# Kernel optimization log

Hardware: AMD Instinct MI355X
Metric: run time of the kernel (lower is better)

## Reference

```python
import jax, jax.numpy as jnp
import numpy as np

N = 2048      # feature_num (nodes/sensors)
T = 5         # timd_num (window length)
D = 64        # embed_dim
TOPK = 21     # topk + 1 (includes self, cos(i,i)=1)
B = 32        # batch
EPS = 1e-5
NEG_SLOPE = 0.2


def setup_inputs() -> dict:
    key = jax.random.key(0)
    ks = jax.random.split(key, 9)
    s = 1.0 / np.sqrt(D)
    return {
        "x": jax.random.normal(ks[0], (B, N, T), jnp.float32),
        "emb": jax.random.normal(ks[1], (N, D), jnp.float32) * s,      # embedding table
        "W": jax.random.normal(ks[2], (D, T), jnp.float32) * (1.0 / np.sqrt(T)),  # GNN lin weight
        "Wb": jax.random.normal(ks[3], (D,), jnp.float32) * 0.01,       # GNN lin bias
        "a_src": jax.random.normal(ks[4], (2 * D,), jnp.float32) * s,   # attention vec (source half)
        "a_dst": jax.random.normal(ks[5], (2 * D,), jnp.float32) * s,   # attention vec (dest half)
        "gamma": jnp.ones((D,), jnp.float32),                            # BatchNorm1d weight
        "beta": jnp.zeros((D,), jnp.float32),                            # BatchNorm1d bias
        "fc_w": jax.random.normal(ks[6], (1, D), jnp.float32) * s,      # fc weight
        "fc_b": jnp.zeros((1,), jnp.float32),                            # fc bias
    }


def reference(x, emb, W, Wb, a_src, a_dst, gamma, beta, fc_w, fc_b):
    # --- cosine-sim topk graph build ---
    norm = jnp.linalg.norm(emb, axis=-1)                    # [N]
    cos = (emb @ emb.T) / (norm[:, None] * norm[None, :])   # [N,N]
    _, idx = jax.lax.top_k(cos, TOPK)                       # [N,TOPK]
    # scatter one-hot adjacency (vectorized, no per-row loop)
    adj = jnp.zeros((N, N), x.dtype).at[jnp.arange(N)[:, None], idx].set(1.0)
    # --- GNN: GDN-style attention message passing ---
    h = jnp.einsum('bnt,dt->bnd', x, W) + Wb                # [B,N,D]
    g = jnp.concatenate([h, jnp.broadcast_to(emb, h.shape)], axis=-1)  # [B,N,2D]
    e_src = g @ a_src                                       # [B,N]
    e_dst = g @ a_dst                                       # [B,N]
    e = jax.nn.leaky_relu(e_src[:, :, None] + e_dst[:, None, :], NEG_SLOPE)  # [B,N,N]
    e = jnp.where(adj > 0, e, jnp.float32(-1e9))
    alpha = jax.nn.softmax(e, axis=-1)                      # [B,N,N], rows sum to 1 over TOPK nbrs
    z = jax.nn.relu(jnp.einsum('bij,bjd->bid', alpha, h))   # [B,N,D]
    # --- output head: z * emb, BN over channels, relu, fc ---
    out = z * emb                                           # [B,N,D]
    mean = out.mean(axis=(0, 1))                            # BN1d stats over (batch, nodes)
    var = out.var(axis=(0, 1))
    out = (out - mean) * jax.lax.rsqrt(var + EPS) * gamma + beta
    out = jax.nn.relu(out)
    out = out @ fc_w.T + fc_b                               # [B,N,1]
    return out.reshape(-1, N)                               # [B,N]
```

## Files before the change

kernel.cpp:

```cpp
#include <hip/hip_runtime.h>
#include <math.h>

#define N_NODES 2048
#define T_WIN 5
#define D_EMB 64
#define TOPK 21
#define B_BATCH 32
#define BN_TOTAL (B_BATCH * N_NODES)
#define EPS_BN 1e-5f
#define NEG_SLOPE 0.2f
#define STATS_STRIDE 16

typedef unsigned long long u64;

__device__ __forceinline__ float wave_sum(float v) {
#pragma unroll
    for (int off = 32; off > 0; off >>= 1) v += __shfl_xor(v, off, 64);
    return v;
}

__device__ __forceinline__ u64 max64(u64 a, u64 b) { return a > b ? a : b; }
__device__ __forceinline__ u64 min64(u64 a, u64 b) { return a < b ? a : b; }

__device__ __forceinline__ u64 bitonic_sort64_desc(u64 key, int lane) {
#pragma unroll
    for (int k = 2; k <= 64; k <<= 1) {
#pragma unroll
        for (int j = k >> 1; j >= 1; j >>= 1) {
            u64 pk = __shfl_xor(key, j, 64);
            bool dirDesc = ((lane & k) == 0);
            bool keepMax = (((lane & j) == 0) == dirDesc);
            key = keepMax ? max64(key, pk) : min64(key, pk);
        }
    }
    return key;
}

__device__ __forceinline__ u64 bitonic_merge_top64(u64 a, u64 b, int lane) {
    u64 br = __shfl(b, 63 - lane, 64);
    u64 c = max64(a, br);
#pragma unroll
    for (int j = 32; j >= 1; j >>= 1) {
        u64 pk = __shfl_xor(c, j, 64);
        bool keepMax = ((lane & j) == 0);
        c = keepMax ? max64(c, pk) : min64(c, pk);
    }
    return c;
}

__global__ __launch_bounds__(256) void k_edge(
    const float* __restrict__ x, const float* __restrict__ W,
    const float* __restrict__ Wb, const float* __restrict__ a_src,
    const float* __restrict__ a_dst, const float* __restrict__ emb,
    float* __restrict__ es2T, float* __restrict__ ed2T,
    float* __restrict__ norms, float* __restrict__ stats,
    float* __restrict__ stats2) {
    if (blockIdx.x < 2) {
        float* p = blockIdx.x ? stats2 : stats;
        ((float4*)p)[threadIdx.x] = make_float4(0.f, 0.f, 0.f, 0.f);
    }
    int wid = threadIdx.x >> 6, lane = threadIdx.x & 63;
    int gw = blockIdx.x * 4 + wid;
    const float* wp = W + lane * T_WIN;
    float w0 = wp[0], w1 = wp[1], w2 = wp[2], w3 = wp[3], w4 = wp[4];
    float bias = Wb[lane];
    float as = a_src[lane], asE = a_src[D_EMB + lane];
    float ad = a_dst[lane], adE = a_dst[D_EMB + lane];

    for (int node = gw; node < BN_TOTAL; node += 8192) {
        int n = node & (N_NODES - 1);
        const float* xp = x + (size_t)node * T_WIN;
        float hv = bias + xp[0] * w0 + xp[1] * w1 + xp[2] * w2 + xp[3] * w3 + xp[4] * w4;
        float e = emb[n * D_EMB + lane];
        if (node < N_NODES) {
            float s2 = wave_sum(e * e);
            if (lane == 0) norms[node] = sqrtf(s2);
        }
        float es = wave_sum(hv * as + e * asE);
        float ed = wave_sum(hv * ad + e * adE);
        if (lane == 0) {
            es2T[node] = es;
            ed2T[node] = ed;
        }
    }
}

__global__ __launch_bounds__(256) void k_gram(
    const float* __restrict__ emb, const float* __restrict__ norms,
    float* __restrict__ cosM) {
    __shared__ __align__(16) float As[64][68];
    __shared__ __align__(16) float Bs[64][68];
    int t = threadIdx.x;
    int g = blockIdx.x;
    int a = (int)((sqrtf(8.f * g + 1.f) - 1.f) * 0.5f);
    while ((a + 1) * (a + 2) / 2 <= g) a++;
    while (a * (a + 1) / 2 > g) a--;
    int bq = g - a * (a + 1) / 2;
    int i0 = a * 64, j0 = bq * 64;

    {
        int r = t >> 2, c0 = t & 3;
        const float4* srcA = (const float4*)(emb + (size_t)(i0 + r) * D_EMB);
        const float4* srcB = (const float4*)(emb + (size_t)(j0 + r) * D_EMB);
#pragma unroll
        for (int k = 0; k < 4; k++) {
            int f4 = c0 + 4 * k;
            float4 v = srcA[f4];
            int d = 4 * f4;
            As[d][r] = v.x; As[d + 1][r] = v.y; As[d + 2][r] = v.z; As[d + 3][r] = v.w;
            float4 w = srcB[f4];
            Bs[d][r] = w.x; Bs[d + 1][r] = w.y; Bs[d + 2][r] = w.z; Bs[d + 3][r] = w.w;
        }
    }
    __syncthreads();

    int ti = t & 15, tj = t >> 4;
    float acc[4][4] = {};
#pragma unroll
    for (int d = 0; d < 64; d++) {
        float4 av = *(const float4*)&As[d][4 * ti];
        float4 bv = *(const float4*)&Bs[d][4 * tj];
        acc[0][0] += av.x * bv.x; acc[0][1] += av.x * bv.y; acc[0][2] += av.x * bv.z; acc[0][3] += av.x * bv.w;
        acc[1][0] += av.y * bv.x; acc[1][1] += av.y * bv.y; acc[1][2] += av.y * bv.z; acc[1][3] += av.y * bv.w;
        acc[2][0] += av.z * bv.x; acc[2][1] += av.z * bv.y; acc[2][2] += av.z * bv.z; acc[2][3] += av.z * bv.w;
        acc[3][0] += av.w * bv.x; acc[3][1] += av.w * bv.y; acc[3][2] += av.w * bv.z; acc[3][3] += av.w * bv.w;
    }

    float nis[4] = {norms[i0 + 4 * ti], norms[i0 + 4 * ti + 1],
                    norms[i0 + 4 * ti + 2], norms[i0 + 4 * ti + 3]};
    float njs[4] = {norms[j0 + 4 * tj], norms[j0 + 4 * tj + 1],
                    norms[j0 + 4 * tj + 2], norms[j0 + 4 * tj + 3]};
#pragma unroll
    for (int r = 0; r < 4; r++) {
        float4 o;
        o.x = acc[r][0] / (nis[r] * njs[0]);
        o.y = acc[r][1] / (nis[r] * njs[1]);
        o.z = acc[r][2] / (nis[r] * njs[2]);
        o.w = acc[r][3] / (nis[r] * njs[3]);
        int i = i0 + 4 * ti + r;
        *(float4*)(cosM + (size_t)i * N_NODES + j0 + 4 * tj) = o;
        cosM[(size_t)(j0 + 4 * tj + 0) * N_NODES + i] = o.x;
        cosM[(size_t)(j0 + 4 * tj + 1) * N_NODES + i] = o.y;
        cosM[(size_t)(j0 + 4 * tj + 2) * N_NODES + i] = o.z;
        cosM[(size_t)(j0 + 4 * tj + 3) * N_NODES + i] = o.w;
    }
}

__global__ __launch_bounds__(256) void k_select(
    const float* __restrict__ cosM, int* __restrict__ idxT) {
    __shared__ u64 candbuf[4][128];
    int tid = threadIdx.x;
    int wid = tid >> 6, lane = tid & 63;
    int i = blockIdx.x * 4 + wid;
    const float* row = cosM + (size_t)i * N_NODES;
    u64* buf = candbuf[wid];

    u64 a = 0;
    u64 t = 0;
    int cnt = 0;
    float vcur = row[lane];

#pragma unroll 1
    for (int c = 0; c < N_NODES / 64; c++) {
        int j = c * 64 + lane;
        float v = vcur;
        if (c < N_NODES / 64 - 1) vcur = row[j + 64];
        unsigned u = __float_as_uint(v);
        u = (u & 0x80000000u) ? ~u : (u | 0x80000000u);
        u64 key = ((u64)u << 32) | (unsigned)(~j);
        unsigned long long ball = __ballot(key > t);
        if (ball) {
            int ofs = __popcll(ball & ((1ull << lane) - 1ull));
            if (key > t) buf[cnt + ofs] = key;
            cnt += (int)__popcll(ball);
            if (cnt >= 64) {
                u64 nk = buf[lane];
                nk = bitonic_sort64_desc(nk, lane);
                a = bitonic_merge_top64(a, nk, lane);
                t = __shfl(a, 20, 64);
                int rem = cnt - 64;
                u64 mv = (lane < rem) ? buf[64 + lane] : 0;
                if (lane < rem) buf[lane] = mv;
                cnt = rem;
            }
        }
    }
    while (cnt > 0) {
        int take = cnt < 64 ? cnt : 64;
        u64 nk = (lane < take) ? buf[lane] : 0;
        nk = bitonic_sort64_desc(nk, lane);
        a = bitonic_merge_top64(a, nk, lane);
        t = __shfl(a, 20, 64);
        int rem = cnt - take;
        u64 mv = (lane < rem) ? buf[take + lane] : 0;
        if (lane < rem) buf[lane] = mv;
        cnt = rem;
    }

    if (lane < TOPK) idxT[lane * N_NODES + i] = (int)(~(unsigned)a);
}

__global__ __launch_bounds__(256) void k_alpha(
    const int* __restrict__ idxT, const float* __restrict__ es2T,
    const float* __restrict__ ed2T, float* __restrict__ alphaT) {
    __shared__ float sed[N_NODES];
    int g = blockIdx.x;
    int b = g & 31;
    int i0 = (g >> 5) * 256;
    int t = threadIdx.x;

    {
        const float4* src = (const float4*)(ed2T + (size_t)b * N_NODES);
        float4* dst = (float4*)sed;
#pragma unroll
        for (int q = 0; q < 2; q++) dst[t + 256 * q] = src[t + 256 * q];
    }
    __syncthreads();

    int i = i0 + t;
    float es = es2T[(size_t)b * N_NODES + i];
    float ev[TOPK];
    float m = -3e38f;
#pragma unroll
    for (int k = 0; k < TOPK; k++) {
        int jk = idxT[k * N_NODES + i];
        float e = es + sed[jk];
        e = e > 0.f ? e : NEG_SLOPE * e;
        ev[k] = e;
        m = fmaxf(m, e);
    }
    float s = 0.f;
#pragma unroll
    for (int k = 0; k < TOPK; k++) {
        ev[k] = __expf(ev[k] - m);
        s += ev[k];
    }
    float inv = 1.0f / s;
#pragma unroll
    for (int k = 0; k < TOPK; k++)
        alphaT[((size_t)b * TOPK + k) * N_NODES + i] = ev[k] * inv;
}

__global__ __launch_bounds__(256, 2) void k_msg(
    const float* __restrict__ x, const float* __restrict__ W,
    const float* __restrict__ Wb, const int* __restrict__ idxT,
    const float* __restrict__ alphaT, const float* __restrict__ emb,
    float* __restrict__ obufT, float* __restrict__ stats,
    float* __restrict__ stats2) {
    __shared__ float hts[N_NODES][6];
    __shared__ float sred[2][4][4];

    int g = blockIdx.x;
    int b = (g & 7) + 8 * ((g >> 3) & 3);
    int c = g >> 5;
    int d0 = c * 4;
    int t = threadIdx.x;
    int wid = t >> 6, lane = t & 63;

    float wc[4][T_WIN], wb4[4];
#pragma unroll
    for (int q = 0; q < 4; q++) {
        wb4[q] = Wb[d0 + q];
#pragma unroll
        for (int tt = 0; tt < T_WIN; tt++) wc[q][tt] = W[(d0 + q) * T_WIN + tt];
    }
    const float* xb = x + (size_t)b * N_NODES * T_WIN;
#pragma unroll
    for (int r = 0; r < 8; r++) {
        int row = t + 256 * r;
        const float* xr = xb + row * T_WIN;
        float x0 = xr[0], x1 = xr[1], x2 = xr[2], x3 = xr[3], x4 = xr[4];
        float h0 = wb4[0] + x0 * wc[0][0] + x1 * wc[0][1] + x2 * wc[0][2] + x3 * wc[0][3] + x4 * wc[0][4];
        float h1 = wb4[1] + x0 * wc[1][0] + x1 * wc[1][1] + x2 * wc[1][2] + x3 * wc[1][3] + x4 * wc[1][4];
        float h2 = wb4[2] + x0 * wc[2][0] + x1 * wc[2][1] + x2 * wc[2][2] + x3 * wc[2][3] + x4 * wc[2][4];
        float h3 = wb4[3] + x0 * wc[3][0] + x1 * wc[3][1] + x2 * wc[3][2] + x3 * wc[3][3] + x4 * wc[3][4];
        *(float2*)&hts[row][0] = make_float2(h0, h1);
        *(float2*)&hts[row][2] = make_float2(h2, h3);
    }
    __syncthreads();

    float sacc[4] = {0.f, 0.f, 0.f, 0.f};
    float sacc2[4] = {0.f, 0.f, 0.f, 0.f};
    const float* aT = alphaT + (size_t)b * TOPK * N_NODES;
#pragma unroll 1
    for (int r = 0; r < 8; r++) {
        int i = 256 * r + t;
        float4 z = make_float4(0.f, 0.f, 0.f, 0.f);
#pragma unroll
        for (int k = 0; k < TOPK; k++) {
            int jk = idxT[k * N_NODES + i];
            float a = aT[(size_t)k * N_NODES + i];
            float2 h01 = *(const float2*)&hts[jk][0];
            float2 h23 = *(const float2*)&hts[jk][2];
            z.x = fmaf(a, h01.x, z.x);
            z.y = fmaf(a, h01.y, z.y);
            z.z = fmaf(a, h23.x, z.z);
            z.w = fmaf(a, h23.y, z.w);
        }
        float4 e4 = *(const float4*)(emb + (size_t)i * D_EMB + d0);
        float4 o;
        o.x = fmaxf(z.x, 0.f) * e4.x;
        o.y = fmaxf(z.y, 0.f) * e4.y;
        o.z = fmaxf(z.z, 0.f) * e4.z;
        o.w = fmaxf(z.w, 0.f) * e4.w;
        ((float4*)obufT)[((size_t)c * B_BATCH + b) * N_NODES + i] = o;
        sacc[0] += o.x; sacc[1] += o.y; sacc[2] += o.z; sacc[3] += o.w;
        sacc2[0] += o.x * o.x; sacc2[1] += o.y * o.y;
        sacc2[2] += o.z * o.z; sacc2[3] += o.w * o.w;
    }

#pragma unroll
    for (int q = 0; q < 4; q++) {
        sacc[q] = wave_sum(sacc[q]);
        sacc2[q] = wave_sum(sacc2[q]);
    }
    if (lane == 0) {
#pragma unroll
        for (int q = 0; q < 4; q++) {
            sred[0][wid][q] = sacc[q];
            sred[1][wid][q] = sacc2[q];
        }
    }
    __syncthreads();
    if (t < 8) {
        int q = t & 3, which = t >> 2;
        float v = sred[which][0][q] + sred[which][1][q] + sred[which][2][q] + sred[which][3][q];
        float* dst = which ? stats2 : stats;
        atomicAdd(&dst[(d0 + q) * STATS_STRIDE], v);
    }
}

__global__ __launch_bounds__(256) void k_out(
    const float* __restrict__ obufT, const float* __restrict__ stats,
    const float* __restrict__ stats2, const float* __restrict__ gamma,
    const float* __restrict__ beta, const float* __restrict__ fc_w,
    const float* __restrict__ fc_b, float* __restrict__ out) {
    int t = threadIdx.x;
    int wid = t >> 6, lane = t & 63;
    int nloc = lane >> 4, c = lane & 15;
    const float invM = 1.0f / (float)BN_TOTAL;

    float mean[4], inv[4], g4[4], bt4[4], fw4[4];
#pragma unroll
    for (int q = 0; q < 4; q++) {
        int d = 4 * c + q;
        float mn = stats[d * STATS_STRIDE] * invM;
        float var = stats2[d * STATS_STRIDE] * invM - mn * mn;
        mean[q] = mn;
        inv[q] = rsqrtf(var + EPS_BN);
        g4[q] = gamma[d]; bt4[q] = beta[d]; fw4[q] = fc_w[d];
    }
    float fb = fc_b[0];

#pragma unroll 1
    for (int r = 0; r < 8; r++) {
        int nd = blockIdx.x * 128 + r * 16 + wid * 4 + nloc;
        int b = nd >> 11, n = nd & (N_NODES - 1);
        float4 o = ((const float4*)obufT)[((size_t)c * B_BATCH + b) * N_NODES + n];
        float p = 0.f;
        float v;
        v = fmaxf((o.x - mean[0]) * inv[0] * g4[0] + bt4[0], 0.f); p = fmaf(v, fw4[0], p);
        v = fmaxf((o.y - mean[1]) * inv[1] * g4[1] + bt4[1], 0.f); p = fmaf(v, fw4[1], p);
        v = fmaxf((o.z - mean[2]) * inv[2] * g4[2] + bt4[2], 0.f); p = fmaf(v, fw4[2], p);
        v = fmaxf((o.w - mean[3]) * inv[3] * g4[3] + bt4[3], 0.f); p = fmaf(v, fw4[3], p);
#pragma unroll
        for (int off = 1; off <= 8; off <<= 1) p += __shfl_xor(p, off, 64);
        if (c == 0) out[nd] = p + fb;
    }
}

extern "C" void kernel_launch(void* const* d_in, const int* in_sizes, int n_in,
                              void* d_out, int out_size, void* d_ws, size_t ws_size,
                              hipStream_t stream) {
    const float* x     = (const float*)d_in[0];
    const float* emb   = (const float*)d_in[1];
    const float* W     = (const float*)d_in[2];
    const float* Wb    = (const float*)d_in[3];
    const float* a_src = (const float*)d_in[4];
    const float* a_dst = (const float*)d_in[5];
    const float* gamma = (const float*)d_in[6];
    const float* beta  = (const float*)d_in[7];
    const float* fc_w  = (const float*)d_in[8];
    const float* fc_b  = (const float*)d_in[9];
    float* out = (float*)d_out;

    char* ws = (char*)d_ws;
    float* stats  = (float*)(ws + 0);
    float* stats2 = (float*)(ws + 4096);
    int*   idxT   = (int*)  (ws + 8192);
    float* norms  = (float*)(ws + 180224);
    float* es2T   = (float*)(ws + 188416);
    float* ed2T   = (float*)(ws + 450560);
    float* alphaT = (float*)(ws + 712704);
    float* cosM   = (float*)(ws + 6217728);
    float* obufT  = cosM;

    k_edge<<<2048, 256, 0, stream>>>(x, W, Wb, a_src, a_dst, emb,
                                     es2T, ed2T, norms, stats, stats2);
    k_gram<<<528, 256, 0, stream>>>(emb, norms, cosM);
    k_select<<<N_NODES / 4, 256, 0, stream>>>(cosM, idxT);
    k_alpha<<<256, 256, 0, stream>>>(idxT, es2T, ed2T, alphaT);
    k_msg<<<512, 256, 0, stream>>>(x, W, Wb, idxT, alphaT, emb, obufT, stats, stats2);
    k_out<<<512, 256, 0, stream>>>(obufT, stats, stats2, gamma, beta, fc_w, fc_b, out);
}
```

Baseline: 152.1 us.

## Fuse edge-score and gram kernels; compute softmax alpha inside message pass

Merges the edge-score kernel into the gram kernel as extra blocks and recomputes row norms in shared memory per tile, which removes a kernel launch and the norms dependency. Drops the separate alpha kernel: the message kernel now stages ed into shared memory and computes the leaky-relu softmax inline, avoiding a global write and read of the alpha array. In exchange, the softmax work is repeated across the 16 channel-group blocks per batch, and the fused kernel uses more registers.

```diff
diff --git a/kernel.cpp b/kernel.cpp
--- a/kernel.cpp
+++ b/kernel.cpp
@@ -48,50 +48,47 @@
     return c;
 }
 
-__global__ __launch_bounds__(256) void k_edge(
-    const float* __restrict__ x, const float* __restrict__ W,
-    const float* __restrict__ Wb, const float* __restrict__ a_src,
-    const float* __restrict__ a_dst, const float* __restrict__ emb,
-    float* __restrict__ es2T, float* __restrict__ ed2T,
-    float* __restrict__ norms, float* __restrict__ stats,
+__global__ __launch_bounds__(256) void k_gram_edge(
+    const float* __restrict__ x, const float* __restrict__ emb,
+    const float* __restrict__ W, const float* __restrict__ Wb,
+    const float* __restrict__ a_src, const float* __restrict__ a_dst,
+    float* __restrict__ cosM, float* __restrict__ es2T,
+    float* __restrict__ ed2T, float* __restrict__ stats,
     float* __restrict__ stats2) {
-    if (blockIdx.x < 2) {
-        float* p = blockIdx.x ? stats2 : stats;
-        ((float4*)p)[threadIdx.x] = make_float4(0.f, 0.f, 0.f, 0.f);
-    }
-    int wid = threadIdx.x >> 6, lane = threadIdx.x & 63;
-    int gw = blockIdx.x * 4 + wid;
-    const float* wp = W + lane * T_WIN;
-    float w0 = wp[0], w1 = wp[1], w2 = wp[2], w3 = wp[3], w4 = wp[4];
-    float bias = Wb[lane];
-    float as = a_src[lane], asE = a_src[D_EMB + lane];
-    float ad = a_dst[lane], adE = a_dst[D_EMB + lane];
-
-    for (int node = gw; node < BN_TOTAL; node += 8192) {
-        int n = node & (N_NODES - 1);
-        const float* xp = x + (size_t)node * T_WIN;
-        float hv = bias + xp[0] * w0 + xp[1] * w1 + xp[2] * w2 + xp[3] * w3 + xp[4] * w4;
-        float e = emb[n * D_EMB + lane];
-        if (node < N_NODES) {
-            float s2 = wave_sum(e * e);
-            if (lane == 0) norms[node] = sqrtf(s2);
-        }
-        float es = wave_sum(hv * as + e * asE);
-        float ed = wave_sum(hv * ad + e * adE);
-        if (lane == 0) {
-            es2T[node] = es;
-            ed2T[node] = ed;
-        }
-    }
-}
-
-__global__ __launch_bounds__(256) void k_gram(
-    const float* __restrict__ emb, const float* __restrict__ norms,
-    float* __restrict__ cosM) {
+    int g = blockIdx.x;
+    int t = threadIdx.x;
+
+    if (g >= 528) {
+        if (g < 530) {
+            float* p = (g == 529) ? stats2 : stats;
+            ((float4*)p)[t] = make_float4(0.f, 0.f, 0.f, 0.f);
+        }
+        int wid = t >> 6, lane = t & 63;
+        int slot = (g - 528) * 4 + wid;
+        const float* wp = W + lane * T_WIN;
+        float w0 = wp[0], w1 = wp[1], w2 = wp[2], w3 = wp[3], w4 = wp[4];
+        float bias = Wb[lane];
+        float as = a_src[lane], asE = a_src[D_EMB + lane];
+        float ad = a_dst[lane], adE = a_dst[D_EMB + lane];
+        for (int node = slot; node < BN_TOTAL; node += 2048) {
+            int n = node & (N_NODES - 1);
+            const float* xp = x + (size_t)node * T_WIN;
+            float hv = bias + xp[0] * w0 + xp[1] * w1 + xp[2] * w2 + xp[3] * w3 + xp[4] * w4;
+            float e = emb[n * D_EMB + lane];
+            float es = wave_sum(hv * as + e * asE);
+            float ed = wave_sum(hv * ad + e * adE);
+            if (lane == 0) {
+                es2T[node] = es;
+                ed2T[node] = ed;
+            }
+        }
+        return;
+    }
+
     __shared__ __align__(16) float As[64][68];
     __shared__ __align__(16) float Bs[64][68];
-    int t = threadIdx.x;
-    int g = blockIdx.x;
+    __shared__ float nIs[64], nJs[64];
+
     int a = (int)((sqrtf(8.f * g + 1.f) - 1.f) * 0.5f);
     while ((a + 1) * (a + 2) / 2 <= g) a++;
     while (a * (a + 1) / 2 > g) a--;
@@ -114,6 +111,20 @@
     }
     __syncthreads();
 
+    if (t < 64) {
+        float s = 0.f;
+#pragma unroll
+        for (int d = 0; d < 64; d++) s += As[d][t] * As[d][t];
+        nIs[t] = sqrtf(s);
+    } else if (t < 128) {
+        int r = t - 64;
+        float s = 0.f;
+#pragma unroll
+        for (int d = 0; d < 64; d++) s += Bs[d][r] * Bs[d][r];
+        nJs[r] = sqrtf(s);
+    }
+    __syncthreads();
+
     int ti = t & 15, tj = t >> 4;
     float acc[4][4] = {};
 #pragma unroll
@@ -126,10 +137,8 @@
         acc[3][0] += av.w * bv.x; acc[3][1] += av.w * bv.y; acc[3][2] += av.w * bv.z; acc[3][3] += av.w * bv.w;
     }
 
-    float nis[4] = {norms[i0 + 4 * ti], norms[i0 + 4 * ti + 1],
-                    norms[i0 + 4 * ti + 2], norms[i0 + 4 * ti + 3]};
-    float njs[4] = {norms[j0 + 4 * tj], norms[j0 + 4 * tj + 1],
-                    norms[j0 + 4 * tj + 2], norms[j0 + 4 * tj + 3]};
+    float nis[4] = {nIs[4 * ti], nIs[4 * ti + 1], nIs[4 * ti + 2], nIs[4 * ti + 3]};
+    float njs[4] = {nJs[4 * tj], nJs[4 * tj + 1], nJs[4 * tj + 2], nJs[4 * tj + 3]};
 #pragma unroll
     for (int r = 0; r < 4; r++) {
         float4 o;
@@ -200,54 +209,14 @@
     if (lane < TOPK) idxT[lane * N_NODES + i] = (int)(~(unsigned)a);
 }
 
-__global__ __launch_bounds__(256) void k_alpha(
-    const int* __restrict__ idxT, const float* __restrict__ es2T,
-    const float* __restrict__ ed2T, float* __restrict__ alphaT) {
-    __shared__ float sed[N_NODES];
-    int g = blockIdx.x;
-    int b = g & 31;
-    int i0 = (g >> 5) * 256;
-    int t = threadIdx.x;
-
-    {
-        const float4* src = (const float4*)(ed2T + (size_t)b * N_NODES);
-        float4* dst = (float4*)sed;
-#pragma unroll
-        for (int q = 0; q < 2; q++) dst[t + 256 * q] = src[t + 256 * q];
-    }
-    __syncthreads();
-
-    int i = i0 + t;
-    float es = es2T[(size_t)b * N_NODES + i];
-    float ev[TOPK];
-    float m = -3e38f;
-#pragma unroll
-    for (int k = 0; k < TOPK; k++) {
-        int jk = idxT[k * N_NODES + i];
-        float e = es + sed[jk];
-        e = e > 0.f ? e : NEG_SLOPE * e;
-        ev[k] = e;
-        m = fmaxf(m, e);
-    }
-    float s = 0.f;
-#pragma unroll
-    for (int k = 0; k < TOPK; k++) {
-        ev[k] = __expf(ev[k] - m);
-        s += ev[k];
-    }
-    float inv = 1.0f / s;
-#pragma unroll
-    for (int k = 0; k < TOPK; k++)
-        alphaT[((size_t)b * TOPK + k) * N_NODES + i] = ev[k] * inv;
-}
-
 __global__ __launch_bounds__(256, 2) void k_msg(
     const float* __restrict__ x, const float* __restrict__ W,
     const float* __restrict__ Wb, const int* __restrict__ idxT,
-    const float* __restrict__ alphaT, const float* __restrict__ emb,
-    float* __restrict__ obufT, float* __restrict__ stats,
-    float* __restrict__ stats2) {
+    const float* __restrict__ es2T, const float* __restrict__ ed2T,
+    const float* __restrict__ emb, float* __restrict__ obufT,
+    float* __restrict__ stats, float* __restrict__ stats2) {
     __shared__ float hts[N_NODES][6];
+    __shared__ float sed[N_NODES];
     __shared__ float sred[2][4][4];
 
     int g = blockIdx.x;
@@ -263,6 +232,12 @@
         wb4[q] = Wb[d0 + q];
 #pragma unroll
         for (int tt = 0; tt < T_WIN; tt++) wc[q][tt] = W[(d0 + q) * T_WIN + tt];
+    }
+    {
+        const float4* src = (const float4*)(ed2T + (size_t)b * N_NODES);
+        float4* dst = (float4*)sed;
+#pragma unroll
+        for (int q = 0; q < 2; q++) dst[t + 256 * q] = src[t + 256 * q];
     }
     const float* xb = x + (size_t)b * N_NODES * T_WIN;
 #pragma unroll
@@ -281,17 +256,34 @@
 
     float sacc[4] = {0.f, 0.f, 0.f, 0.f};
     float sacc2[4] = {0.f, 0.f, 0.f, 0.f};
-    const float* aT = alphaT + (size_t)b * TOPK * N_NODES;
 #pragma unroll 1
     for (int r = 0; r < 8; r++) {
         int i = 256 * r + t;
+        float es = es2T[(size_t)b * N_NODES + i];
+        int jk[TOPK];
+        float ev[TOPK];
+        float m = -3e38f;
+#pragma unroll
+        for (int k = 0; k < TOPK; k++) {
+            jk[k] = idxT[k * N_NODES + i];
+            float e = es + sed[jk[k]];
+            e = e > 0.f ? e : NEG_SLOPE * e;
+            ev[k] = e;
+            m = fmaxf(m, e);
+        }
+        float s = 0.f;
+#pragma unroll
+        for (int k = 0; k < TOPK; k++) {
+            ev[k] = __expf(ev[k] - m);
+            s += ev[k];
+        }
+        float inv = 1.0f / s;
         float4 z = make_float4(0.f, 0.f, 0.f, 0.f);
 #pragma unroll
         for (int k = 0; k < TOPK; k++) {
-            int jk = idxT[k * N_NODES + i];
-            float a = aT[(size_t)k * N_NODES + i];
-            float2 h01 = *(const float2*)&hts[jk][0];
-            float2 h23 = *(const float2*)&hts[jk][2];
+            float a = ev[k] * inv;
+            float2 h01 = *(const float2*)&hts[jk[k]][0];
+            float2 h23 = *(const float2*)&hts[jk[k]][2];
             z.x = fmaf(a, h01.x, z.x);
             z.y = fmaf(a, h01.y, z.y);
             z.z = fmaf(a, h23.x, z.z);
@@ -388,18 +380,16 @@
     float* stats  = (float*)(ws + 0);
     float* stats2 = (float*)(ws + 4096);
     int*   idxT   = (int*)  (ws + 8192);
-    float* norms  = (float*)(ws + 180224);
-    float* es2T   = (float*)(ws + 188416);
-    float* ed2T   = (float*)(ws + 450560);
-    float* alphaT = (float*)(ws + 712704);
-    float* cosM   = (float*)(ws + 6217728);
+    float* es2T   = (float*)(ws + 180224);
+    float* ed2T   = (float*)(ws + 442368);
+    float* cosM   = (float*)(ws + 704512);
     float* obufT  = cosM;
 
-    k_edge<<<2048, 256, 0, stream>>>(x, W, Wb, a_src, a_dst, emb,
-                                     es2T, ed2T, norms, stats, stats2);
-    k_gram<<<528, 256, 0, stream>>>(emb, norms, cosM);
+    k_gram_edge<<<1040, 256, 0, stream>>>(x, emb, W, Wb, a_src, a_dst,
+                                          cosM, es2T, ed2T, stats, stats2);
     k_select<<<N_NODES / 4, 256, 0, stream>>>(cosM, idxT);
-    k_alpha<<<256, 256, 0, stream>>>(idxT, es2T, ed2T, alphaT);
-    k_msg<<<512, 256, 0, stream>>>(x, W, Wb, idxT, alphaT, emb, obufT, stats, stats2);
-    k_out<<<512, 256, 0, stream>>>(obufT, stats, stats2, gamma, beta, fc_w, fc_b, out);
-}
+    k_msg<<<512, 256, 0, stream>>>(x, W, Wb, idxT, es2T, ed2T, emb,
+                                   obufT, stats, stats2);
+    k_out<<<512, 256, 0, stream>>>(obufT, stats, stats2, gamma, beta,
+                                   fc_w, fc_b, out);
+}
```

Result: slower. 156.1 us (+2.7%).
